# Performance work log

Hardware: AMD Instinct MI355X
Metric: run time of the kernel (lower is better)

Reference implementation:

```python
import jax, jax.numpy as jnp
import numpy as np

B, P, C, F = 16, 1000, 91, 1024      # images, proposals/img, classes (incl bg), box-head dim
H, W = 800, 800                      # image shape (all images same size)
SCORE_THRESH = 0.05
NMS_THRESH = 0.5
DETS = 100                           # detections_per_img
MIN_SIZE = 1e-2
BBOX_XFORM_CLIP = float(np.log(1000.0 / 16.0))
OFF = float(max(H, W) + 2)           # class offset unit for batched (class-aware) NMS


def setup_inputs() -> dict:
    key = jax.random.key(0)
    k1, k2, k3, k4 = jax.random.split(key, 4)
    box_features = jax.random.normal(k1, (B * P, F), jnp.float32)
    Wc = jax.random.normal(k2, (F, C), jnp.float32) * 0.02
    bc = jnp.zeros((C,), jnp.float32)
    Wb = jax.random.normal(k3, (F, C * 4), jnp.float32) * 0.02
    bb = jnp.zeros((C * 4,), jnp.float32)
    u = jax.random.uniform(k4, (B, P, 4), jnp.float32)
    x1 = u[..., 0] * (W * 0.8)
    y1 = u[..., 1] * (H * 0.8)
    x2 = x1 + 16.0 + u[..., 2] * (W * 0.2)
    y2 = y1 + 16.0 + u[..., 3] * (H * 0.2)
    proposals = jnp.stack([x1, y1, x2, y2], axis=-1)
    return dict(box_features=box_features, Wc=Wc, bc=bc, Wb=Wb, bb=bb,
                proposals=proposals)


def _decode_and_clip(regs, props):
    # regs: [N, C, 4] deltas; props: [N, 4] xyxy. bbox_reg_weights = (1,1,1,1).
    w = props[:, 2] - props[:, 0]
    h = props[:, 3] - props[:, 1]
    cx = props[:, 0] + 0.5 * w
    cy = props[:, 1] + 0.5 * h
    dx, dy = regs[..., 0], regs[..., 1]
    dw = jnp.minimum(regs[..., 2], BBOX_XFORM_CLIP)
    dh = jnp.minimum(regs[..., 3], BBOX_XFORM_CLIP)
    pcx = dx * w[:, None] + cx[:, None]
    pcy = dy * h[:, None] + cy[:, None]
    pw = jnp.exp(dw) * w[:, None]
    ph = jnp.exp(dh) * h[:, None]
    x1 = jnp.clip(pcx - 0.5 * pw, 0.0, float(W))
    y1 = jnp.clip(pcy - 0.5 * ph, 0.0, float(H))
    x2 = jnp.clip(pcx + 0.5 * pw, 0.0, float(W))
    y2 = jnp.clip(pcy + 0.5 * ph, 0.0, float(H))
    return jnp.stack([x1, y1, x2, y2], axis=-1)  # [N, C, 4]


def _iou_one_vs_all(box, boxes):
    ix1 = jnp.maximum(box[0], boxes[:, 0])
    iy1 = jnp.maximum(box[1], boxes[:, 1])
    ix2 = jnp.minimum(box[2], boxes[:, 2])
    iy2 = jnp.minimum(box[3], boxes[:, 3])
    inter = jnp.clip(ix2 - ix1, 0.0) * jnp.clip(iy2 - iy1, 0.0)
    a1 = (box[2] - box[0]) * (box[3] - box[1])
    a2 = (boxes[:, 2] - boxes[:, 0]) * (boxes[:, 3] - boxes[:, 1])
    return inter / (a1 + a2 - inter + 1e-9)


def _greedy_nms(boxes, scores):
    # boxes: [M,4] (class-offset), scores: [M] (-inf = filtered out).
    # Returns selected indices [DETS] and scores [DETS] (0 where no valid pick).
    def body(i, st):
        sc, sel, ss = st
        j = jnp.argmax(sc)
        s = sc[j]
        iou = _iou_one_vs_all(boxes[j], boxes)
        sc = jnp.where(iou > NMS_THRESH, -jnp.inf, sc)  # suppresses j itself too
        valid = s > 0.0
        sel = sel.at[i].set(jnp.where(valid, j.astype(jnp.int32), 0))
        ss = ss.at[i].set(jnp.where(valid, s, 0.0))
        return sc, sel, ss
    init = (scores, jnp.zeros((DETS,), jnp.int32), jnp.zeros((DETS,), jnp.float32))
    _, sel, ss = jax.lax.fori_loop(0, DETS, body, init)
    return sel, ss


def reference(box_features, Wc, bc, Wb, bb, proposals):
    # Box predictor (FastRCNNPredictor-style linear heads).
    class_logits = box_features @ Wc + bc                  # [B*P, C]
    box_regression = (box_features @ Wb + bb).reshape(-1, C, 4)
    # Decode per-class boxes against proposals, clip to image.
    pred = _decode_and_clip(box_regression, proposals.reshape(-1, 4))  # [B*P, C, 4]
    scores = jax.nn.softmax(class_logits, axis=-1)         # [B*P, C]
    # Drop background class 0; flatten (proposal, class) per image.
    M = P * (C - 1)
    boxes_all = pred[:, 1:, :].reshape(B, M, 4)
    scores_all = scores[:, 1:].reshape(B, M)
    labels_all = jnp.tile(jnp.arange(1, C, dtype=jnp.int32), P)  # [M]
    # Score threshold + remove tiny boxes (mask instead of dynamic filter).
    bw = boxes_all[..., 2] - boxes_all[..., 0]
    bh = boxes_all[..., 3] - boxes_all[..., 1]
    keep = (scores_all > SCORE_THRESH) & (bw >= MIN_SIZE) & (bh >= MIN_SIZE)
    scores_m = jnp.where(keep, scores_all, -jnp.inf)
    # Class-aware batched NMS via per-class coordinate offsets.
    boxes_off = boxes_all + (labels_all.astype(jnp.float32) * OFF)[None, :, None]
    sel, det_scores = jax.vmap(_greedy_nms)(boxes_off, scores_m)   # [B,DETS]
    det_boxes = jnp.take_along_axis(boxes_all, sel[..., None], axis=1)  # [B,DETS,4]
    det_labels = labels_all[sel]                                        # [B,DETS]
    valid = det_scores > 0.0
    det_boxes = det_boxes * valid[..., None]
    det_labels = jnp.where(valid, det_labels, 0)
    return det_boxes, det_scores, det_labels
```

## Files before the change

### kernel.cpp

```cpp
#include <hip/hip_runtime.h>
#include <hip/hip_bf16.h>
#include <math.h>

typedef unsigned long long ull;
typedef __attribute__((ext_vector_type(8))) short bf16x8;
typedef __attribute__((ext_vector_type(4))) float f32x4;

#define BB_ 16
#define PP_ 1000
#define CC_ 91
#define FF_ 1024
#define DETS_ 100
#define CAP_ 2048
#define CAND_MAX (BB_ * CAP_)
#define SURV_CAP 2048
#define CLS_CAP 256
#define BLK_CAND 720
#define IMG_W 800.0f
#define IMG_H 800.0f
#define OFF_ 802.0f
#define SCORE_TH 0.05f
#define PRE_TH 0.042f
#define NMS_TH 0.5f
#define MIN_SZ 0.01f
#define BBOX_CLIP_D 4.135166556742356

__global__ __launch_bounds__(256) void wb_transpose(
    const float* __restrict__ Wb, float* __restrict__ Wbt)
{
    const int idx = blockIdx.x * 256 + threadIdx.x;
    if (idx >= CC_ * 4 * FF_) return;
    const int c = idx >> 12;
    const int j = (idx >> 10) & 3;
    const int k = idx & 1023;
    if (c < 1) { Wbt[idx] = 0.f; return; }
    Wbt[idx] = Wb[(size_t)k * (CC_ * 4) + 4 * c + j];
}

__global__ __launch_bounds__(256) void wc_bf16_t(
    const float* __restrict__ Wc, ushort* __restrict__ Wct)
{
    const int idx = blockIdx.x * 256 + threadIdx.x;
    if (idx >= 96 * FF_) return;
    const int c = idx >> 10, k = idx & 1023;
    const float v = (c < CC_) ? Wc[(size_t)k * CC_ + c] : 0.f;
    const unsigned u = __float_as_uint(v);
    Wct[idx] = (ushort)((u + 0x8000u) >> 16);
}

__global__ __launch_bounds__(256) void prepass_mfma(
    const float* __restrict__ A, const ushort* __restrict__ Wct,
    const float* __restrict__ bc,
    int* __restrict__ rowlist, int* __restrict__ nrowsp)
{
    __shared__ union __align__(16) SM {
        struct { ushort As[32][40]; ushort Bt[96][40]; } t;
        float Ssc[32][97];
    } sm;

    const int tid = threadIdx.x;
    const int row0 = blockIdx.x * 32;
    const int lane = tid & 63;
    const int w = tid >> 6;
    const int rowOff = (w & 1) * 16;
    const int colOff = (w >> 1) * 48;

    const int arow = tid >> 3;
    const int ak4 = (tid & 7) * 4;
    const int bcol = tid >> 1;
    const int bkh = (tid & 1) * 16;

    f32x4 acc0 = {0.f, 0.f, 0.f, 0.f};
    f32x4 acc1 = {0.f, 0.f, 0.f, 0.f};
    f32x4 acc2 = {0.f, 0.f, 0.f, 0.f};

    float4 avP = *(const float4*)(A + (size_t)(row0 + arow) * FF_ + ak4);
    uint4 bvP0 = make_uint4(0, 0, 0, 0), bvP1 = make_uint4(0, 0, 0, 0);
    if (tid < 192) {
        const ushort* src = Wct + (size_t)bcol * FF_ + bkh;
        bvP0 = *(const uint4*)(src);
        bvP1 = *(const uint4*)(src + 8);
    }

    for (int k0 = 0; k0 < FF_; k0 += 32) {
        {
            const unsigned b0 = __float_as_uint(avP.x), b1 = __float_as_uint(avP.y);
            const unsigned b2 = __float_as_uint(avP.z), b3 = __float_as_uint(avP.w);
            const unsigned u0 = ((b0 + 0x8000u) >> 16) | (((b1 + 0x8000u) >> 16) << 16);
            const unsigned u1 = ((b2 + 0x8000u) >> 16) | (((b3 + 0x8000u) >> 16) << 16);
            *(uint2*)&sm.t.As[arow][ak4] = make_uint2(u0, u1);
        }
        if (tid < 192) {
            *(uint4*)&sm.t.Bt[bcol][bkh] = bvP0;
            *(uint4*)&sm.t.Bt[bcol][bkh + 8] = bvP1;
        }

        const int kn = k0 + 32;
        if (kn < FF_) {
            avP = *(const float4*)(A + (size_t)(row0 + arow) * FF_ + kn + ak4);
            if (tid < 192) {
                const ushort* src = Wct + (size_t)bcol * FF_ + kn + bkh;
                bvP0 = *(const uint4*)(src);
                bvP1 = *(const uint4*)(src + 8);
            }
        }
        __syncthreads();

        const bf16x8 aF  = *(const bf16x8*)&sm.t.As[rowOff + (lane & 15)][(lane >> 4) * 8];
        const bf16x8 bF0 = *(const bf16x8*)&sm.t.Bt[colOff +  0 + (lane & 15)][(lane >> 4) * 8];
        const bf16x8 bF1 = *(const bf16x8*)&sm.t.Bt[colOff + 16 + (lane & 15)][(lane >> 4) * 8];
        const bf16x8 bF2 = *(const bf16x8*)&sm.t.Bt[colOff + 32 + (lane & 15)][(lane >> 4) * 8];
        acc0 = __builtin_amdgcn_mfma_f32_16x16x32_bf16(aF, bF0, acc0, 0, 0, 0);
        acc1 = __builtin_amdgcn_mfma_f32_16x16x32_bf16(aF, bF1, acc1, 0, 0, 0);
        acc2 = __builtin_amdgcn_mfma_f32_16x16x32_bf16(aF, bF2, acc2, 0, 0, 0);
        __syncthreads();
    }

    {
        const int r0 = rowOff + (lane >> 4) * 4;
        const int cb = colOff + (lane & 15);
#pragma unroll
        for (int reg = 0; reg < 4; ++reg) {
            const int row = r0 + reg;
            int c = cb;
            if (c < CC_) sm.Ssc[row][c] = acc0[reg] + bc[c];
            c = cb + 16;
            if (c < CC_) sm.Ssc[row][c] = acc1[reg] + bc[c];
            c = cb + 32;
            if (c < CC_) sm.Ssc[row][c] = acc2[reg] + bc[c];
        }
    }
    __syncthreads();

    if (tid < 32) {
        float m_all = sm.Ssc[tid][0];
        float m_fg = -INFINITY;
        for (int c = 1; c < CC_; ++c) {
            const float lv = sm.Ssc[tid][c];
            m_all = fmaxf(m_all, lv);
            m_fg = fmaxf(m_fg, lv);
        }
        float denom = 0.f;
        for (int c = 0; c < CC_; ++c) denom += expf(sm.Ssc[tid][c] - m_all);
        const float maxsc = expf(m_fg - m_all) / denom;
        if (maxsc > PRE_TH) {
            const int pos = atomicAdd(nrowsp, 1);
            rowlist[pos] = row0 + tid;
        }
    }
}

template<bool USE_T>
__global__ __launch_bounds__(512) void logits_fp64_rows(
    const float* __restrict__ A, const float* __restrict__ Wc,
    const float* __restrict__ bc,
    const float* __restrict__ Wb, const float* __restrict__ Wbt,
    const float* __restrict__ bb, const float* __restrict__ props,
    const int* __restrict__ rowlist, const int* __restrict__ nrowsp,
    float* __restrict__ cs, int* __restrict__ clab,
    int* __restrict__ corig, int* __restrict__ cpidx,
    int* __restrict__ cnt,
    float* __restrict__ cx1, float* __restrict__ cy1,
    float* __restrict__ cx2, float* __restrict__ cy2)
{
    const int nr = *nrowsp;
    const int row0 = blockIdx.x * 8;
    if (row0 >= nr) return;

    __shared__ union __align__(16) SM {
        struct { float Af[2][16][12]; float Bs[2][16][98]; } t;
        struct { int cp[BLK_CAND]; int cc[BLK_CAND]; int cg[BLK_CAND]; } d;
    } sm;
    __shared__ __align__(16) double dcomb[256][3];
    __shared__ float Ssc[8][97];
    __shared__ int ncand;

    const int tid = threadIdx.x;
    const int kg = tid >> 8;
    const int l = tid & 255;
    const int kbase = kg * 512;
    const int r = l >> 5;
    const int c0 = (l & 31) * 3;

    if (tid == 0) ncand = 0;

    const int aslot = l >> 2;
    const int akq = (l & 3) * 4;
    const float* Arow = nullptr;
    if (l < 32) {
        const int ridx = min(row0 + aslot, nr - 1);
        Arow = A + (size_t)rowlist[ridx] * FF_ + kbase;
    }
    const int bk = l >> 4;
    const int bn = (l & 15) * 6;

    double acc[3] = {0.0, 0.0, 0.0};

    float4 avP = make_float4(0.f, 0.f, 0.f, 0.f);
    if (l < 32) avP = *reinterpret_cast<const float4*>(Arow + akq);
    float bvP[6];
#pragma unroll
    for (int jj = 0; jj < 6; ++jj) {
        const int c = bn + jj;
        bvP[jj] = (c < CC_) ? Wc[(size_t)(kbase + bk) * CC_ + c] : 0.f;
    }

    for (int k0 = 0; k0 < 512; k0 += 16) {
        if (l < 32) {
            sm.t.Af[kg][akq + 0][aslot] = avP.x;
            sm.t.Af[kg][akq + 1][aslot] = avP.y;
            sm.t.Af[kg][akq + 2][aslot] = avP.z;
            sm.t.Af[kg][akq + 3][aslot] = avP.w;
        }
#pragma unroll
        for (int jj = 0; jj < 6; ++jj) sm.t.Bs[kg][bk][bn + jj] = bvP[jj];

        const int kn = k0 + 16;
        if (kn < 512) {
            if (l < 32)
                avP = *reinterpret_cast<const float4*>(Arow + kn + akq);
#pragma unroll
            for (int jj = 0; jj < 6; ++jj) {
                const int c = bn + jj;
                bvP[jj] = (c < CC_) ? Wc[(size_t)(kbase + kn + bk) * CC_ + c] : 0.f;
            }
        }
        __syncthreads();

#pragma unroll
        for (int k = 0; k < 16; ++k) {
            const double a0 = (double)sm.t.Af[kg][k][r];
            const double b0 = (double)sm.t.Bs[kg][k][c0 + 0];
            const double b1 = (double)sm.t.Bs[kg][k][c0 + 1];
            const double b2 = (double)sm.t.Bs[kg][k][c0 + 2];
            acc[0] += a0 * b0;
            acc[1] += a0 * b1;
            acc[2] += a0 * b2;
        }
        __syncthreads();
    }

    if (kg == 1) {
#pragma unroll
        for (int j = 0; j < 3; ++j) dcomb[l][j] = acc[j];
    }
    __syncthreads();
    if (kg == 0) {
#pragma unroll
        for (int j = 0; j < 3; ++j) {
            const int c = c0 + j;
            if (c < CC_) {
                const double v = acc[j] + dcomb[l][j];
                Ssc[r][c] = __fadd_rn((float)v, bc[c]);
            }
        }
    }
    __syncthreads();

    {
        const int w = tid >> 6;
        const int lane = tid & 63;
        if (w < 8 && row0 + w < nr) {
            const int p = rowlist[row0 + w];
            const int b = p / PP_;
            const int pi = p - b * PP_;

            const float l1 = Ssc[w][lane];
            const float l2 = (lane < CC_ - 64) ? Ssc[w][lane + 64] : -INFINITY;
            float m = fmaxf(l1, l2);
#pragma unroll
            for (int off = 32; off > 0; off >>= 1)
                m = fmaxf(m, __shfl_xor(m, off));

            double d = exp((double)l1 - (double)m);
            if (lane < CC_ - 64) d += exp((double)l2 - (double)m);
#pragma unroll
            for (int off = 1; off < 64; off <<= 1)
                d += __shfl_xor(d, off);

#pragma unroll
            for (int q = 0; q < 2; ++q) {
                const int c = lane + q * 64;
                if (c >= 1 && c < CC_) {
                    const double sd = exp((double)Ssc[w][c] - (double)m) / d;
                    const float score = (float)sd;
                    if (score > SCORE_TH) {
                        const int pos = atomicAdd(&cnt[b], 1);
                        if (pos < CAP_) {
                            const int g = b * CAP_ + pos;
                            cs[g] = score;
                            clab[g] = c;
                            corig[g] = pi * (CC_ - 1) + (c - 1);
                            cpidx[g] = p;
                            const int slot = atomicAdd(&ncand, 1);
                            if (slot < BLK_CAND) {
                                sm.d.cp[slot] = p;
                                sm.d.cc[slot] = c;
                                sm.d.cg[slot] = g;
                            }
                        }
                    }
                }
            }
        }
    }
    __syncthreads();

    {
        const int w = tid >> 6;
        const int lane = tid & 63;
        const int nc = min(ncand, BLK_CAND);
        for (int ci = w; ci < nc; ci += 8) {
            const int p = sm.d.cp[ci];
            const int c = sm.d.cc[ci];
            const int g = sm.d.cg[ci];

            const float* fr = A + (size_t)p * FF_;
            double a0 = 0.0, a1 = 0.0, a2 = 0.0, a3 = 0.0;
            if (USE_T) {
                const float* w0 = Wbt + (size_t)c * 4096;
                for (int k = lane; k < FF_; k += 64) {
                    const double f = (double)fr[k];
                    a0 += f * (double)w0[k];
                    a1 += f * (double)w0[1024 + k];
                    a2 += f * (double)w0[2048 + k];
                    a3 += f * (double)w0[3072 + k];
                }
            } else {
                const float* wb0 = Wb + 4 * c;
                for (int k = lane; k < FF_; k += 64) {
                    const double f = (double)fr[k];
                    const float4 wv = *reinterpret_cast<const float4*>(
                        wb0 + (size_t)k * (CC_ * 4));
                    a0 += f * (double)wv.x; a1 += f * (double)wv.y;
                    a2 += f * (double)wv.z; a3 += f * (double)wv.w;
                }
            }
#pragma unroll
            for (int off = 32; off > 0; off >>= 1) {
                a0 += __shfl_xor(a0, off);
                a1 += __shfl_xor(a1, off);
                a2 += __shfl_xor(a2, off);
                a3 += __shfl_xor(a3, off);
            }

            if (lane == 0) {
                const float dx = __fadd_rn((float)a0, bb[4 * c + 0]);
                const float dy = __fadd_rn((float)a1, bb[4 * c + 1]);
                const float clipf = (float)BBOX_CLIP_D;
                const float dw = fminf(__fadd_rn((float)a2, bb[4 * c + 2]), clipf);
                const float dh = fminf(__fadd_rn((float)a3, bb[4 * c + 3]), clipf);

                const float px1 = props[(size_t)p * 4 + 0];
                const float py1 = props[(size_t)p * 4 + 1];
                const float px2 = props[(size_t)p * 4 + 2];
                const float py2 = props[(size_t)p * 4 + 3];
                const float wq = __fsub_rn(px2, px1);
                const float hq = __fsub_rn(py2, py1);
                const float cxq = __fadd_rn(px1, __fmul_rn(0.5f, wq));
                const float cyq = __fadd_rn(py1, __fmul_rn(0.5f, hq));

                const float pcx = __fadd_rn(__fmul_rn(dx, wq), cxq);
                const float pcy = __fadd_rn(__fmul_rn(dy, hq), cyq);
                const float ew = (float)exp((double)dw);
                const float eh = (float)exp((double)dh);
                const float pw = __fmul_rn(ew, wq);
                const float ph = __fmul_rn(eh, hq);

                const float hw = __fmul_rn(0.5f, pw);
                const float hh = __fmul_rn(0.5f, ph);
                const float bx1 = fminf(fmaxf(__fsub_rn(pcx, hw), 0.f), IMG_W);
                const float by1 = fminf(fmaxf(__fsub_rn(pcy, hh), 0.f), IMG_H);
                const float bx2 = fminf(fmaxf(__fadd_rn(pcx, hw), 0.f), IMG_W);
                const float by2 = fminf(fmaxf(__fadd_rn(pcy, hh), 0.f), IMG_H);

                cx1[g] = bx1; cy1[g] = by1; cx2[g] = bx2; cy2[g] = by2;
                if (!(__fsub_rn(bx2, bx1) >= MIN_SZ && __fsub_rn(by2, by1) >= MIN_SZ)) {
                    cs[g] = -INFINITY;
                }
            }
        }
    }
}

__global__ __launch_bounds__(64) void nms_class(
    const float* __restrict__ c_x1, const float* __restrict__ c_y1,
    const float* __restrict__ c_x2, const float* __restrict__ c_y2,
    const float* __restrict__ c_s, const int* __restrict__ c_lab,
    const int* __restrict__ c_orig, const int* __restrict__ cnt,
    ull* __restrict__ skey, float* __restrict__ sx1v, float* __restrict__ sy1v,
    float* __restrict__ sx2v, float* __restrict__ sy2v,
    int* __restrict__ slabv, int* __restrict__ scnt)
{
    const int blk = blockIdx.x;
    const int b = blk / (CC_ - 1);
    const int c = 1 + (blk - b * (CC_ - 1));
    const int lane = threadIdx.x;

    __shared__ ull kk[CLS_CAP];
    __shared__ float x1s[CLS_CAP], y1s[CLS_CAP], x2s[CLS_CAP], y2s[CLS_CAP];

    const int n = min(cnt[b], CAP_);

    int mcnt = 0;
    for (int i0 = 0; i0 < n; i0 += 64) {
        const int i = i0 + lane;
        bool take = false;
        float s = 0.f; int so = 0; int g = 0;
        if (i < n) {
            g = b * CAP_ + i;
            if (c_lab[g] == c) {
                s = c_s[g];
                if (s > 0.f) { take = true; so = c_orig[g]; }
            }
        }
        const ull bal = __ballot(take);
        if (take) {
            const int pos = mcnt + __popcll(bal & ((1ull << lane) - 1ull));
            if (pos < CLS_CAP) {
                kk[pos] = ((ull)__float_as_uint(s) << 32) |
                          (unsigned int)(0x7FFFFFFF - so);
                x1s[pos] = c_x1[g]; y1s[pos] = c_y1[g];
                x2s[pos] = c_x2[g]; y2s[pos] = c_y2[g];
            }
        }
        mcnt += (int)__popcll(bal);
    }
    mcnt = min(mcnt, CLS_CAP);
    if (mcnt == 0) return;
    __syncthreads();

    while (true) {
        ull best = 0ull;
        for (int i = lane; i < mcnt; i += 64) best = (kk[i] > best) ? kk[i] : best;
#pragma unroll
        for (int off = 32; off > 0; off >>= 1) {
            const ull o = __shfl_xor(best, off);
            best = (o > best) ? o : best;
        }
        if (best == 0ull) break;

        int wsl = -1;
        for (int i = lane; i < mcnt; i += 64) if (kk[i] == best) wsl = i;
        const ull bal = __ballot(wsl >= 0);
        const int wlane = (int)__ffsll((long long)bal) - 1;
        wsl = __shfl(wsl, wlane);

        const float wx1 = x1s[wsl], wy1 = y1s[wsl];
        const float wx2 = x2s[wsl], wy2 = y2s[wsl];

        if (lane == 0) {
            const int sp = atomicAdd(&scnt[b], 1);
            if (sp < SURV_CAP) {
                const int sg = b * SURV_CAP + sp;
                skey[sg] = best;
                sx1v[sg] = wx1; sy1v[sg] = wy1;
                sx2v[sg] = wx2; sy2v[sg] = wy2;
                slabv[sg] = c;
            }
        }

        const float off = __fmul_rn((float)c, OFF_);
        const float ax1 = __fadd_rn(wx1, off), ay1 = __fadd_rn(wy1, off);
        const float ax2 = __fadd_rn(wx2, off), ay2 = __fadd_rn(wy2, off);
        const float a1 = __fmul_rn(__fsub_rn(ax2, ax1), __fsub_rn(ay2, ay1));
        for (int i = lane; i < mcnt; i += 64) {
            if (kk[i] == 0ull) continue;
            const float bx1 = __fadd_rn(x1s[i], off), by1 = __fadd_rn(y1s[i], off);
            const float bx2 = __fadd_rn(x2s[i], off), by2 = __fadd_rn(y2s[i], off);
            const float ix1 = fmaxf(ax1, bx1), iy1 = fmaxf(ay1, by1);
            const float ix2 = fminf(ax2, bx2), iy2 = fminf(ay2, by2);
            const float inter = __fmul_rn(fmaxf(__fsub_rn(ix2, ix1), 0.f),
                                          fmaxf(__fsub_rn(iy2, iy1), 0.f));
            const float a2 = __fmul_rn(__fsub_rn(bx2, bx1), __fsub_rn(by2, by1));
            const float den = __fadd_rn(__fsub_rn(__fadd_rn(a1, a2), inter), 1e-9f);
            const float iou = __fdiv_rn(inter, den);
            if (iou > NMS_TH) kk[i] = 0ull;
        }
        __syncthreads();
    }
}

__global__ __launch_bounds__(256) void nms_merge(
    const ull* __restrict__ skey, const float* __restrict__ sx1v,
    const float* __restrict__ sy1v, const float* __restrict__ sx2v,
    const float* __restrict__ sy2v, const int* __restrict__ slabv,
    const int* __restrict__ scnt, float* __restrict__ out)
{
    const int b = blockIdx.x;
    const int t = threadIdx.x;

    __shared__ ull k_[SURV_CAP];
    __shared__ int id_[SURV_CAP];

    const int m = min(scnt[b], SURV_CAP);
    int N2 = 128;
    while (N2 < m) N2 <<= 1;

    for (int i = t; i < N2; i += 256) {
        k_[i] = (i < m) ? skey[b * SURV_CAP + i] : 0ull;
        id_[i] = i;
    }
    __syncthreads();

    for (int ksz = 2; ksz <= N2; ksz <<= 1) {
        for (int j = ksz >> 1; j > 0; j >>= 1) {
            for (int i = t; i < N2; i += 256) {
                const int ixj = i ^ j;
                if (ixj > i) {
                    const ull a = k_[i], cc = k_[ixj];
                    const bool desc = ((i & ksz) == 0);
                    if (desc ? (a < cc) : (a > cc)) {
                        k_[i] = cc; k_[ixj] = a;
                        const int tmp = id_[i]; id_[i] = id_[ixj]; id_[ixj] = tmp;
                    }
                }
            }
            __syncthreads();
        }
    }

    const int boxes_base = 0;
    const int scores_base = BB_ * DETS_ * 4;
    const int labels_base = BB_ * DETS_ * 5;

    for (int r = t; r < DETS_; r += 256) {
        const ull key = (r < N2) ? k_[r] : 0ull;
        float* bo = out + boxes_base + (size_t)(b * DETS_ + r) * 4;
        if (key != 0ull) {
            const int sg = b * SURV_CAP + id_[r];
            bo[0] = sx1v[sg]; bo[1] = sy1v[sg];
            bo[2] = sx2v[sg]; bo[3] = sy2v[sg];
            out[scores_base + b * DETS_ + r] = __uint_as_float((unsigned)(key >> 32));
            out[labels_base + b * DETS_ + r] = (float)slabv[sg];
        } else {
            bo[0] = 0.f; bo[1] = 0.f; bo[2] = 0.f; bo[3] = 0.f;
            out[scores_base + b * DETS_ + r] = 0.f;
            out[labels_base + b * DETS_ + r] = 0.f;
        }
    }
}

extern "C" void kernel_launch(void* const* d_in, const int* in_sizes, int n_in,
                              void* d_out, int out_size, void* d_ws, size_t ws_size,
                              hipStream_t stream)
{
    const float* feat  = (const float*)d_in[0];
    const float* Wc    = (const float*)d_in[1];
    const float* bc    = (const float*)d_in[2];
    const float* Wb    = (const float*)d_in[3];
    const float* bb    = (const float*)d_in[4];
    const float* props = (const float*)d_in[5];
    for (int i = 0; i < n_in; ++i) {
        const float* q = (const float*)d_in[i];
        switch (in_sizes[i]) {
            case 16384000: feat  = q; break;
            case 93184:    Wc    = q; break;
            case 91:       bc    = q; break;
            case 372736:   Wb    = q; break;
            case 364:      bb    = q; break;
            case 64000:    props = q; break;
        }
    }
    float* out = (float*)d_out;

    char* ws = (char*)d_ws;
    int*   cnt    = (int*)ws;
    int*   scnt   = (int*)(ws + 64);
    int*   nrowsp = (int*)(ws + 128);
    float* cs    = (float*)(ws + 256);
    int*   clab  = (int*)(cs + CAND_MAX);
    int*   corig = clab + CAND_MAX;
    int*   cpidx = corig + CAND_MAX;
    float* cx1   = (float*)(cpidx + CAND_MAX);
    float* cy1   = cx1 + CAND_MAX;
    float* cx2   = cy1 + CAND_MAX;
    float* cy2   = cx2 + CAND_MAX;
    ull*   skey  = (ull*)(cy2 + CAND_MAX);
    float* sx1v  = (float*)(skey + (size_t)BB_ * SURV_CAP);
    float* sy1v  = sx1v + (size_t)BB_ * SURV_CAP;
    float* sx2v  = sy1v + (size_t)BB_ * SURV_CAP;
    float* sy2v  = sx2v + (size_t)BB_ * SURV_CAP;
    int*   slabv = (int*)(sy2v + (size_t)BB_ * SURV_CAP);
    int*   rowlist = slabv + (size_t)BB_ * SURV_CAP;
    ushort* Wct  = (ushort*)(rowlist + 16384);
    float* Wbt   = (float*)(Wct + 96 * FF_);

    const size_t need = ((char*)(Wbt + CC_ * 4 * FF_)) - ws;
    const bool useT = (ws_size >= need);

    hipMemsetAsync(ws, 0, 256, stream);

    wc_bf16_t<<<(96 * FF_ + 255) / 256, 256, 0, stream>>>(Wc, Wct);
    if (useT)
        wb_transpose<<<(CC_ * 4 * FF_ + 255) / 256, 256, 0, stream>>>(Wb, Wbt);

    prepass_mfma<<<BB_ * PP_ / 32, 256, 0, stream>>>(feat, Wct, bc,
        rowlist, nrowsp);

    if (useT)
        logits_fp64_rows<true><<<BB_ * PP_ / 8, 512, 0, stream>>>(
            feat, Wc, bc, Wb, Wbt, bb, props, rowlist, nrowsp,
            cs, clab, corig, cpidx, cnt, cx1, cy1, cx2, cy2);
    else
        logits_fp64_rows<false><<<BB_ * PP_ / 8, 512, 0, stream>>>(
            feat, Wc, bc, Wb, Wbt, bb, props, rowlist, nrowsp,
            cs, clab, corig, cpidx, cnt, cx1, cy1, cx2, cy2);

    nms_class<<<BB_ * (CC_ - 1), 64, 0, stream>>>(
        cx1, cy1, cx2, cy2, cs, clab, corig, cnt,
        skey, sx1v, sy1v, sx2v, sy2v, slabv, scnt);

    nms_merge<<<BB_, 256, 0, stream>>>(
        skey, sx1v, sy1v, sx2v, sy2v, slabv, scnt, out);
}
```

Baseline: 251.0 us.

## Use split-bf16 (hi/lo) MFMA prepass to tighten score prefilter threshold

The bf16 prepass that decides which rows need exact fp64 logits now splits both features and class weights into high and low bf16 parts and accumulates three MFMA products. This makes the approximate scores accurate enough that the prefilter threshold can move closer to the real score threshold (0.042 to 0.048). Fewer rows are then sent to the expensive fp64 logits kernel. The cost is triple the MFMA work plus extra shared memory and weight traffic in the prepass, and a risk of missing borderline rows if the error bound is wrong.

```diff
diff --git a/kernel.cpp b/kernel.cpp
--- a/kernel.cpp
+++ b/kernel.cpp
@@ -20,10 +20,14 @@
 #define IMG_H 800.0f
 #define OFF_ 802.0f
 #define SCORE_TH 0.05f
-#define PRE_TH 0.042f
+#define PRE_TH 0.048f
 #define NMS_TH 0.5f
 #define MIN_SZ 0.01f
 #define BBOX_CLIP_D 4.135166556742356
+
+__device__ __forceinline__ ushort bf16_hi(float v) {
+    return (ushort)((__float_as_uint(v) + 0x8000u) >> 16);
+}
 
 __global__ __launch_bounds__(256) void wb_transpose(
     const float* __restrict__ Wb, float* __restrict__ Wbt)
@@ -37,24 +41,28 @@
     Wbt[idx] = Wb[(size_t)k * (CC_ * 4) + 4 * c + j];
 }
 
-__global__ __launch_bounds__(256) void wc_bf16_t(
-    const float* __restrict__ Wc, ushort* __restrict__ Wct)
+__global__ __launch_bounds__(256) void wc_bf16_split(
+    const float* __restrict__ Wc, ushort* __restrict__ Wcth,
+    ushort* __restrict__ Wctl)
 {
     const int idx = blockIdx.x * 256 + threadIdx.x;
     if (idx >= 96 * FF_) return;
     const int c = idx >> 10, k = idx & 1023;
     const float v = (c < CC_) ? Wc[(size_t)k * CC_ + c] : 0.f;
-    const unsigned u = __float_as_uint(v);
-    Wct[idx] = (ushort)((u + 0x8000u) >> 16);
+    const ushort h = bf16_hi(v);
+    const float hf = __uint_as_float(((unsigned)h) << 16);
+    Wcth[idx] = h;
+    Wctl[idx] = bf16_hi(v - hf);
 }
 
 __global__ __launch_bounds__(256) void prepass_mfma(
-    const float* __restrict__ A, const ushort* __restrict__ Wct,
-    const float* __restrict__ bc,
+    const float* __restrict__ A, const ushort* __restrict__ Wcth,
+    const ushort* __restrict__ Wctl, const float* __restrict__ bc,
     int* __restrict__ rowlist, int* __restrict__ nrowsp)
 {
     __shared__ union __align__(16) SM {
-        struct { ushort As[32][40]; ushort Bt[96][40]; } t;
+        struct { ushort Ah[32][40]; ushort Al[32][40];
+                 ushort Bh[96][40]; ushort Bl[96][40]; } t;
         float Ssc[32][97];
     } sm;
 
@@ -75,44 +83,65 @@
     f32x4 acc2 = {0.f, 0.f, 0.f, 0.f};
 
     float4 avP = *(const float4*)(A + (size_t)(row0 + arow) * FF_ + ak4);
-    uint4 bvP0 = make_uint4(0, 0, 0, 0), bvP1 = make_uint4(0, 0, 0, 0);
+    uint4 bhP0 = make_uint4(0,0,0,0), bhP1 = make_uint4(0,0,0,0);
+    uint4 blP0 = make_uint4(0,0,0,0), blP1 = make_uint4(0,0,0,0);
     if (tid < 192) {
-        const ushort* src = Wct + (size_t)bcol * FF_ + bkh;
-        bvP0 = *(const uint4*)(src);
-        bvP1 = *(const uint4*)(src + 8);
+        const ushort* sh = Wcth + (size_t)bcol * FF_ + bkh;
+        const ushort* sl = Wctl + (size_t)bcol * FF_ + bkh;
+        bhP0 = *(const uint4*)(sh);  bhP1 = *(const uint4*)(sh + 8);
+        blP0 = *(const uint4*)(sl);  blP1 = *(const uint4*)(sl + 8);
     }
 
     for (int k0 = 0; k0 < FF_; k0 += 32) {
         {
-            const unsigned b0 = __float_as_uint(avP.x), b1 = __float_as_uint(avP.y);
-            const unsigned b2 = __float_as_uint(avP.z), b3 = __float_as_uint(avP.w);
-            const unsigned u0 = ((b0 + 0x8000u) >> 16) | (((b1 + 0x8000u) >> 16) << 16);
-            const unsigned u1 = ((b2 + 0x8000u) >> 16) | (((b3 + 0x8000u) >> 16) << 16);
-            *(uint2*)&sm.t.As[arow][ak4] = make_uint2(u0, u1);
+            float vv[4] = {avP.x, avP.y, avP.z, avP.w};
+            ushort hh[4], ll[4];
+#pragma unroll
+            for (int j = 0; j < 4; ++j) {
+                hh[j] = bf16_hi(vv[j]);
+                const float hf = __uint_as_float(((unsigned)hh[j]) << 16);
+                ll[j] = bf16_hi(vv[j] - hf);
+            }
+            *(uint2*)&sm.t.Ah[arow][ak4] = make_uint2(
+                (unsigned)hh[0] | ((unsigned)hh[1] << 16),
+                (unsigned)hh[2] | ((unsigned)hh[3] << 16));
+            *(uint2*)&sm.t.Al[arow][ak4] = make_uint2(
+                (unsigned)ll[0] | ((unsigned)ll[1] << 16),
+                (unsigned)ll[2] | ((unsigned)ll[3] << 16));
         }
         if (tid < 192) {
-            *(uint4*)&sm.t.Bt[bcol][bkh] = bvP0;
-            *(uint4*)&sm.t.Bt[bcol][bkh + 8] = bvP1;
+            *(uint4*)&sm.t.Bh[bcol][bkh]     = bhP0;
+            *(uint4*)&sm.t.Bh[bcol][bkh + 8] = bhP1;
+            *(uint4*)&sm.t.Bl[bcol][bkh]     = blP0;
+            *(uint4*)&sm.t.Bl[bcol][bkh + 8] = blP1;
         }
 
         const int kn = k0 + 32;
         if (kn < FF_) {
             avP = *(const float4*)(A + (size_t)(row0 + arow) * FF_ + kn + ak4);
             if (tid < 192) {
-                const ushort* src = Wct + (size_t)bcol * FF_ + kn + bkh;
-                bvP0 = *(const uint4*)(src);
-                bvP1 = *(const uint4*)(src + 8);
+                const ushort* sh = Wcth + (size_t)bcol * FF_ + kn + bkh;
+                const ushort* sl = Wctl + (size_t)bcol * FF_ + kn + bkh;
+                bhP0 = *(const uint4*)(sh);  bhP1 = *(const uint4*)(sh + 8);
+                blP0 = *(const uint4*)(sl);  blP1 = *(const uint4*)(sl + 8);
             }
         }
         __syncthreads();
 
-        const bf16x8 aF  = *(const bf16x8*)&sm.t.As[rowOff + (lane & 15)][(lane >> 4) * 8];
-        const bf16x8 bF0 = *(const bf16x8*)&sm.t.Bt[colOff +  0 + (lane & 15)][(lane >> 4) * 8];
-        const bf16x8 bF1 = *(const bf16x8*)&sm.t.Bt[colOff + 16 + (lane & 15)][(lane >> 4) * 8];
-        const bf16x8 bF2 = *(const bf16x8*)&sm.t.Bt[colOff + 32 + (lane & 15)][(lane >> 4) * 8];
-        acc0 = __builtin_amdgcn_mfma_f32_16x16x32_bf16(aF, bF0, acc0, 0, 0, 0);
-        acc1 = __builtin_amdgcn_mfma_f32_16x16x32_bf16(aF, bF1, acc1, 0, 0, 0);
-        acc2 = __builtin_amdgcn_mfma_f32_16x16x32_bf16(aF, bF2, acc2, 0, 0, 0);
+        const int ar = rowOff + (lane & 15);
+        const int ke = (lane >> 4) * 8;
+        const bf16x8 aH = *(const bf16x8*)&sm.t.Ah[ar][ke];
+        const bf16x8 aL = *(const bf16x8*)&sm.t.Al[ar][ke];
+#pragma unroll
+        for (int ct = 0; ct < 3; ++ct) {
+            const int bc_ = colOff + ct * 16 + (lane & 15);
+            const bf16x8 bH = *(const bf16x8*)&sm.t.Bh[bc_][ke];
+            const bf16x8 bL = *(const bf16x8*)&sm.t.Bl[bc_][ke];
+            f32x4* acc = (ct == 0) ? &acc0 : (ct == 1) ? &acc1 : &acc2;
+            *acc = __builtin_amdgcn_mfma_f32_16x16x32_bf16(aH, bH, *acc, 0, 0, 0);
+            *acc = __builtin_amdgcn_mfma_f32_16x16x32_bf16(aH, bL, *acc, 0, 0, 0);
+            *acc = __builtin_amdgcn_mfma_f32_16x16x32_bf16(aL, bH, *acc, 0, 0, 0);
+        }
         __syncthreads();
     }
 
@@ -583,19 +612,20 @@
     float* sy2v  = sx2v + (size_t)BB_ * SURV_CAP;
     int*   slabv = (int*)(sy2v + (size_t)BB_ * SURV_CAP);
     int*   rowlist = slabv + (size_t)BB_ * SURV_CAP;
-    ushort* Wct  = (ushort*)(rowlist + 16384);
-    float* Wbt   = (float*)(Wct + 96 * FF_);
+    ushort* Wcth = (ushort*)(rowlist + 16384);
+    ushort* Wctl = Wcth + 96 * FF_;
+    float* Wbt   = (float*)(Wctl + 96 * FF_);
 
     const size_t need = ((char*)(Wbt + CC_ * 4 * FF_)) - ws;
     const bool useT = (ws_size >= need);
 
     hipMemsetAsync(ws, 0, 256, stream);
 
-    wc_bf16_t<<<(96 * FF_ + 255) / 256, 256, 0, stream>>>(Wc, Wct);
+    wc_bf16_split<<<(96 * FF_ + 255) / 256, 256, 0, stream>>>(Wc, Wcth, Wctl);
     if (useT)
         wb_transpose<<<(CC_ * 4 * FF_ + 255) / 256, 256, 0, stream>>>(Wb, Wbt);
 
-    prepass_mfma<<<BB_ * PP_ / 32, 256, 0, stream>>>(feat, Wct, bc,
+    prepass_mfma<<<BB_ * PP_ / 32, 256, 0, stream>>>(feat, Wcth, Wctl, bc,
         rowlist, nrowsp);
 
     if (useT)
```

New measurement: 240.3 us. 1.04x faster.
